# Kernel optimization log

Hardware: AMD Instinct MI355X
Metric: run time of the kernel (lower is better)

The kernel has to match this reference:

```python
import jax, jax.numpy as jnp
import numpy as np

N_NODES = 100000
N_EDGES = 1600000
D_IN = 64
D_OUT = 64
NUM_ETYPE = 2
NEG_SLOPE = 0.2


def setup_inputs() -> dict:
    key = jax.random.key(0)
    ks = jax.random.split(key, 9)
    feat = jax.random.normal(ks[0], (N_NODES, D_IN), dtype=jnp.float32)
    rel = jax.random.uniform(ks[1], (N_EDGES, NUM_ETYPE), dtype=jnp.float32)
    W_self = jax.random.normal(ks[2], (D_OUT, D_IN), dtype=jnp.float32) * 0.1
    b_self = jax.random.normal(ks[3], (D_OUT,), dtype=jnp.float32) * 0.1
    W_neigh = jax.random.normal(ks[4], (D_OUT, D_IN), dtype=jnp.float32) * 0.1
    b_neigh = jax.random.normal(ks[5], (D_OUT,), dtype=jnp.float32) * 0.1
    attn_e = jax.random.normal(ks[6], (NUM_ETYPE, 1), dtype=jnp.float32)
    src = jax.random.randint(ks[7], (N_EDGES,), 0, N_NODES, dtype=jnp.int32)
    dst = jax.random.randint(ks[8], (N_EDGES,), 0, N_NODES, dtype=jnp.int32)
    return {"feat": feat, "rel": rel, "W_self": W_self, "b_self": b_self,
            "W_neigh": W_neigh, "b_neigh": b_neigh, "attn_e": attn_e,
            "src": src, "dst": dst}


def reference(feat, rel, W_self, b_self, W_neigh, b_neigh, attn_e, src, dst):
    n = feat.shape[0]
    # per-edge attention score: [E, num_etype] @ [num_etype, 1] -> [E]
    e = jnp.squeeze(rel @ attn_e, axis=1)
    e = jax.nn.leaky_relu(e, negative_slope=NEG_SLOPE)
    # edge_softmax: segment softmax over edges grouped by destination node
    emax = jax.ops.segment_max(e, dst, num_segments=n)          # [N]
    ex = jnp.exp(e - emax[dst])                                  # [E]
    denom = jax.ops.segment_sum(ex, dst, num_segments=n)        # [N]
    a = ex / denom[dst]                                          # [E]
    # u_mul_e + sum aggregation: neigh[v] = sum_e a_e * feat[src_e]
    m = feat[src] * a[:, None]                                   # [E, D_IN]
    h_neigh = jax.ops.segment_sum(m, dst, num_segments=n)       # [N, D_IN]
    # rst = fc_self(h_self) + fc_neigh(h_neigh)  (torch Linear: x @ W.T + b)
    return feat @ W_self.T + b_self + h_neigh @ W_neigh.T + b_neigh
```

## Files before the change

### kernel.cpp

```cpp
#include <hip/hip_runtime.h>
#include <hip/hip_bf16.h>

#define N_NODES 100000
#define N_EDGES 1600000
#define D 64
#define NEG_SLOPE 0.2f

#define BSHIFT 10
#define BNODES 1024
#define NBUCK ((N_NODES + BNODES - 1) >> BSHIFT)
#define BUCKET_CAP 17408
#define P1_EPB 4096
#define P1_T 512
#define P1_IT (P1_EPB / P1_T)

__global__ __launch_bounds__(P1_T) void binning_kernel(
    const float2* __restrict__ rel, const float* __restrict__ attn_e,
    const int* __restrict__ src, const int* __restrict__ dst,
    int* __restrict__ bucket_cursor, uint2* __restrict__ binned)
{
    __shared__ uint2 staged1[P1_EPB];
    __shared__ uint2 staged2[P1_EPB];
    __shared__ int cnt[NBUCK];
    __shared__ int excl[NBUCK];
    __shared__ int chunkbase[NBUCK];

    int tid = threadIdx.x;
    int e0 = blockIdx.x * P1_EPB;
    int n = min(P1_EPB, N_EDGES - e0);

    for (int b = tid; b < NBUCK; b += P1_T) cnt[b] = 0;
    __syncthreads();

    float a0 = attn_e[0], a1 = attn_e[1];

    int myslot[P1_IT];
    #pragma unroll
    for (int j = 0; j < P1_IT; ++j) {
        int i = tid + j * P1_T;
        if (i < n) {
            int e = e0 + i;
            float2 r = rel[e];
            float sc = r.x * a0 + r.y * a1;
            sc = (sc > 0.f) ? sc : NEG_SLOPE * sc;
            float ev = __expf(sc);
            unsigned u = __float_as_uint(ev) + 0x8000u;
            unsigned wcode = (u >> 16) & 0x7FFFu;
            unsigned s = (unsigned)src[e];
            unsigned d = (unsigned)dst[e];
            staged1[i] = make_uint2((s << 15) | wcode, d);
            myslot[j] = atomicAdd(&cnt[d >> BSHIFT], 1);
        }
    }
    __syncthreads();
    if (tid == 0) {
        int run = 0;
        for (int b = 0; b < NBUCK; ++b) { excl[b] = run; run += cnt[b]; }
    }
    __syncthreads();
    #pragma unroll
    for (int j = 0; j < P1_IT; ++j) {
        int i = tid + j * P1_T;
        if (i < n) {
            uint2 v = staged1[i];
            staged2[excl[v.y >> BSHIFT] + myslot[j]] = v;
        }
    }
    if (tid < NBUCK)
        chunkbase[tid] = atomicAdd(&bucket_cursor[tid], cnt[tid]);
    __syncthreads();
    for (int i = tid; i < n; i += P1_T) {
        uint2 v = staged2[i];
        int b = (int)(v.y >> BSHIFT);
        binned[(size_t)b * BUCKET_CAP + chunkbase[b] + (i - excl[b])] = v;
    }
}

__global__ __launch_bounds__(1024) void csr_kernel(
    const int* __restrict__ bucket_cursor, const uint2* __restrict__ binned,
    int* __restrict__ offsets, unsigned* __restrict__ edata)
{
    __shared__ unsigned vals[BUCKET_CAP];
    __shared__ int hist[BNODES];
    __shared__ int nexcl[BNODES];
    __shared__ int cur[BNODES];
    __shared__ int bc[NBUCK];
    __shared__ int base_sh;

    int b = blockIdx.x;
    int tid = threadIdx.x;

    if (tid < NBUCK) bc[tid] = bucket_cursor[tid];
    hist[tid] = 0;
    cur[tid] = 0;
    __syncthreads();
    if (tid == 0) {
        int s = 0;
        for (int i = 0; i < b; ++i) s += bc[i];
        base_sh = s;
    }
    __syncthreads();
    int count = bc[b];
    int base = base_sh;
    const uint2* bin = binned + (size_t)b * BUCKET_CAP;

    for (int i = tid; i < count; i += 1024)
        atomicAdd(&hist[bin[i].y & (BNODES - 1)], 1);
    __syncthreads();

    int h = hist[tid];
    nexcl[tid] = h;
    __syncthreads();
    for (int d = 1; d < BNODES; d <<= 1) {
        int u = (tid >= d) ? nexcl[tid - d] : 0;
        __syncthreads();
        nexcl[tid] += u;
        __syncthreads();
    }
    int excl = nexcl[tid] - h;
    __syncthreads();
    nexcl[tid] = excl;
    __syncthreads();

    int node = (b << BSHIFT) + tid;
    if (node < N_NODES) offsets[node] = base + excl;
    if (b == NBUCK - 1 && tid == 0) offsets[N_NODES] = N_EDGES;

    for (int i = tid; i < count; i += 1024) {
        uint2 e = bin[i];
        int d = e.y & (BNODES - 1);
        int t = atomicAdd(&cur[d], 1);
        vals[nexcl[d] + t] = e.x;
    }
    __syncthreads();
    for (int i = tid; i < count; i += 1024)
        edata[base + i] = vals[i];
}

typedef __attribute__((ext_vector_type(8))) short bf16x8;
typedef __attribute__((ext_vector_type(4))) float f32x4;
#define MFMA16(a, b, c) __builtin_amdgcn_mfma_f32_16x16x32_bf16(a, b, c, 0, 0, 0)

__device__ __forceinline__ short bf16_rne(float f) {
    unsigned u = __float_as_uint(f);
    u += 0x7FFFu + ((u >> 16) & 1u);
    return (short)(u >> 16);
}
__device__ __forceinline__ float bf16_to_f(short h) {
    return __uint_as_float(((unsigned)(unsigned short)h) << 16);
}
__device__ __forceinline__ void cvt8(float4 f0, float4 f1,
                                     bf16x8& hi, bf16x8& lo) {
    float v[8] = {f0.x, f0.y, f0.z, f0.w, f1.x, f1.y, f1.z, f1.w};
    #pragma unroll
    for (int j = 0; j < 8; ++j) {
        short h = bf16_rne(v[j]);
        hi[j] = h;
        lo[j] = bf16_rne(v[j] - bf16_to_f(h));
    }
}

__global__ __launch_bounds__(512) void gemm_fused_kernel(
    const float* __restrict__ feat, const float* __restrict__ W_self,
    const float* __restrict__ W_neigh, const float* __restrict__ b_self,
    const float* __restrict__ b_neigh, float* __restrict__ out,
    __hip_bfloat16* __restrict__ g)
{
    int tid = threadIdx.x;
    int lane = tid & 63;
    int wave = tid >> 6;
    int llo = lane & 15;
    int lhi = lane >> 4;
    int rb = blockIdx.x * 128 + wave * 16;
    if (rb >= N_NODES) return;

    int arow = rb + llo;
    if (arow > N_NODES - 1) arow = N_NODES - 1;
    const float4* fr = (const float4*)(feat + (size_t)arow * D);
    bf16x8 ahi[2], alo[2];
    #pragma unroll
    for (int s = 0; s < 2; ++s)
        cvt8(fr[s * 8 + lhi * 2], fr[s * 8 + lhi * 2 + 1], ahi[s], alo[s]);

    unsigned short* g16 = (unsigned short*)g;
    #pragma unroll
    for (int nt = 0; nt < 4; ++nt) {
        int col = nt * 16 + llo;
        const float4* ws = (const float4*)(W_self + (size_t)col * D);
        const float4* wn = (const float4*)(W_neigh + (size_t)col * D);
        f32x4 accS = {0.f, 0.f, 0.f, 0.f};
        f32x4 accN = {0.f, 0.f, 0.f, 0.f};
        #pragma unroll
        for (int s = 0; s < 2; ++s) {
            bf16x8 bh, bl;
            cvt8(ws[s * 8 + lhi * 2], ws[s * 8 + lhi * 2 + 1], bh, bl);
            accS = MFMA16(ahi[s], bh, accS);
            accS = MFMA16(alo[s], bh, accS);
            accS = MFMA16(ahi[s], bl, accS);
            cvt8(wn[s * 8 + lhi * 2], wn[s * 8 + lhi * 2 + 1], bh, bl);
            accN = MFMA16(ahi[s], bh, accN);
            accN = MFMA16(alo[s], bh, accN);
            accN = MFMA16(ahi[s], bl, accN);
        }
        float bias = b_self[col] + b_neigh[col];
        #pragma unroll
        for (int rg = 0; rg < 4; ++rg) {
            int r = rb + lhi * 4 + rg;
            if (r < N_NODES) {
                out[(size_t)r * D + col] = accS[rg] + bias;
                g16[(size_t)r * D + col] = (unsigned short)bf16_rne(accN[rg]);
            }
        }
    }
}

__global__ __launch_bounds__(256) void aggregate_kernel(
    const uint* __restrict__ g32, const unsigned* __restrict__ edata,
    const int* __restrict__ offsets, float* __restrict__ out)
{
    int v = blockIdx.x * 4 + (threadIdx.x >> 6);
    int lane = threadIdx.x & 63;
    int q = lane >> 4;
    int t = lane & 15;
    int lo = offsets[v], hi = offsets[v + 1];
    float4 acc = make_float4(0.f, 0.f, 0.f, 0.f);
    float sum = 0.f;

    for (int i = lo; i < hi; i += 16) {
        int e0 = i + q;
        int e1 = i + 4 + q;
        int e2 = i + 8 + q;
        int e3 = i + 12 + q;
        int ec0 = (e0 < hi) ? e0 : hi - 1;
        int ec1 = (e1 < hi) ? e1 : hi - 1;
        int ec2 = (e2 < hi) ? e2 : hi - 1;
        int ec3 = (e3 < hi) ? e3 : hi - 1;
        unsigned p0 = edata[ec0];
        unsigned p1 = edata[ec1];
        unsigned p2 = edata[ec2];
        unsigned p3 = edata[ec3];
        float w0 = (e0 < hi) ? __uint_as_float((p0 & 0x7FFFu) << 16) : 0.f;
        float w1 = (e1 < hi) ? __uint_as_float((p1 & 0x7FFFu) << 16) : 0.f;
        float w2 = (e2 < hi) ? __uint_as_float((p2 & 0x7FFFu) << 16) : 0.f;
        float w3 = (e3 < hi) ? __uint_as_float((p3 & 0x7FFFu) << 16) : 0.f;
        const uint2* r0 = (const uint2*)(g32 + (size_t)(p0 >> 15) * (D / 2));
        const uint2* r1 = (const uint2*)(g32 + (size_t)(p1 >> 15) * (D / 2));
        const uint2* r2 = (const uint2*)(g32 + (size_t)(p2 >> 15) * (D / 2));
        const uint2* r3 = (const uint2*)(g32 + (size_t)(p3 >> 15) * (D / 2));
        uint2 u0 = r0[t];
        uint2 u1 = r1[t];
        uint2 u2 = r2[t];
        uint2 u3 = r3[t];
        acc.x += w0 * __uint_as_float(u0.x << 16);
        acc.y += w0 * __uint_as_float(u0.x & 0xFFFF0000u);
        acc.z += w0 * __uint_as_float(u0.y << 16);
        acc.w += w0 * __uint_as_float(u0.y & 0xFFFF0000u);
        sum += w0;
        acc.x += w1 * __uint_as_float(u1.x << 16);
        acc.y += w1 * __uint_as_float(u1.x & 0xFFFF0000u);
        acc.z += w1 * __uint_as_float(u1.y << 16);
        acc.w += w1 * __uint_as_float(u1.y & 0xFFFF0000u);
        sum += w1;
        acc.x += w2 * __uint_as_float(u2.x << 16);
        acc.y += w2 * __uint_as_float(u2.x & 0xFFFF0000u);
        acc.z += w2 * __uint_as_float(u2.y << 16);
        acc.w += w2 * __uint_as_float(u2.y & 0xFFFF0000u);
        sum += w2;
        acc.x += w3 * __uint_as_float(u3.x << 16);
        acc.y += w3 * __uint_as_float(u3.x & 0xFFFF0000u);
        acc.z += w3 * __uint_as_float(u3.y << 16);
        acc.w += w3 * __uint_as_float(u3.y & 0xFFFF0000u);
        sum += w3;
    }
    #pragma unroll
    for (int mm = 16; mm <= 32; mm <<= 1) {
        acc.x += __shfl_xor(acc.x, mm, 64);
        acc.y += __shfl_xor(acc.y, mm, 64);
        acc.z += __shfl_xor(acc.z, mm, 64);
        acc.w += __shfl_xor(acc.w, mm, 64);
        sum   += __shfl_xor(sum,   mm, 64);
    }
    if (hi > lo && q == 0) {
        float inv = 1.f / sum;
        float4* orow = (float4*)(out + (size_t)v * D);
        float4 c = orow[t];
        c.x += acc.x * inv; c.y += acc.y * inv;
        c.z += acc.z * inv; c.w += acc.w * inv;
        orow[t] = c;
    }
}

extern "C" void kernel_launch(void* const* d_in, const int* in_sizes, int n_in,
                              void* d_out, int out_size, void* d_ws, size_t ws_size,
                              hipStream_t stream) {
    const float* feat    = (const float*)d_in[0];
    const float* rel     = (const float*)d_in[1];
    const float* W_self  = (const float*)d_in[2];
    const float* b_self  = (const float*)d_in[3];
    const float* W_neigh = (const float*)d_in[4];
    const float* b_neigh = (const float*)d_in[5];
    const float* attn_e  = (const float*)d_in[6];
    const int*   src     = (const int*)d_in[7];
    const int*   dst     = (const int*)d_in[8];
    float* out = (float*)d_out;

    uint2* binned = (uint2*)d_ws;
    __hip_bfloat16* g = (__hip_bfloat16*)(binned + (size_t)NBUCK * BUCKET_CAP);
    unsigned* edata = (unsigned*)((char*)g + (size_t)N_NODES * D * 2);
    int* offsets = (int*)(edata + N_EDGES);
    int* bucket_cursor = offsets + N_NODES + 1;

    hipMemsetAsync(bucket_cursor, 0, NBUCK * sizeof(int), stream);

    binning_kernel<<<(N_EDGES + P1_EPB - 1) / P1_EPB, P1_T, 0, stream>>>(
        (const float2*)rel, attn_e, src, dst, bucket_cursor, binned);
    csr_kernel<<<NBUCK, 1024, 0, stream>>>(
        bucket_cursor, binned, offsets, edata);
    gemm_fused_kernel<<<(N_NODES + 127) / 128, 512, 0, stream>>>(
        feat, W_self, W_neigh, b_self, b_neigh, out, g);
    aggregate_kernel<<<N_NODES / 4, 256, 0, stream>>>(
        (const uint*)g, edata, offsets, out);
}
```

Before: 206.8 us.

## Precompute bf16 weight fragments once, transpose GEMM output mapping, shrink CSR buckets

An extra block in the binning kernel converts W_self and W_neigh into hi/lo bf16 MFMA fragments a single time and sums the two biases into one vector. Before this, every GEMM wave reloaded and converted the weights itself. The GEMM swaps the MFMA operand roles so each lane holds four consecutive output columns of one node, which lets it write float4 and packed bf16 stores instead of scalar ones. It also halves the block size. Separately, the bucket size drops from 1024 to 512 nodes, giving the CSR kernel more blocks, each with less shared memory. The cost is that only half the threads do work in the CSR prefix scan.

Result: faster. 189.8 us (-8.2%).

```diff
diff --git a/kernel.cpp b/kernel.cpp
--- a/kernel.cpp
+++ b/kernel.cpp
@@ -6,18 +6,45 @@
 #define D 64
 #define NEG_SLOPE 0.2f
 
-#define BSHIFT 10
-#define BNODES 1024
+#define BSHIFT 9
+#define BNODES 512
 #define NBUCK ((N_NODES + BNODES - 1) >> BSHIFT)
-#define BUCKET_CAP 17408
+#define BUCKET_CAP 8896
 #define P1_EPB 4096
 #define P1_T 512
 #define P1_IT (P1_EPB / P1_T)
+#define GRID_BIN ((N_EDGES + P1_EPB - 1) / P1_EPB)
+
+typedef __attribute__((ext_vector_type(8))) short bf16x8;
+typedef __attribute__((ext_vector_type(4))) float f32x4;
+#define MFMA16(a, b, c) __builtin_amdgcn_mfma_f32_16x16x32_bf16(a, b, c, 0, 0, 0)
+
+__device__ __forceinline__ short bf16_rne(float f) {
+    unsigned u = __float_as_uint(f);
+    u += 0x7FFFu + ((u >> 16) & 1u);
+    return (short)(u >> 16);
+}
+__device__ __forceinline__ float bf16_to_f(short h) {
+    return __uint_as_float(((unsigned)(unsigned short)h) << 16);
+}
+__device__ __forceinline__ void cvt8(float4 f0, float4 f1,
+                                     bf16x8& hi, bf16x8& lo) {
+    float v[8] = {f0.x, f0.y, f0.z, f0.w, f1.x, f1.y, f1.z, f1.w};
+    #pragma unroll
+    for (int j = 0; j < 8; ++j) {
+        short h = bf16_rne(v[j]);
+        hi[j] = h;
+        lo[j] = bf16_rne(v[j] - bf16_to_f(h));
+    }
+}
 
 __global__ __launch_bounds__(P1_T) void binning_kernel(
     const float2* __restrict__ rel, const float* __restrict__ attn_e,
     const int* __restrict__ src, const int* __restrict__ dst,
-    int* __restrict__ bucket_cursor, uint2* __restrict__ binned)
+    int* __restrict__ bucket_cursor, uint2* __restrict__ binned,
+    const float* __restrict__ W_self, const float* __restrict__ W_neigh,
+    const float* __restrict__ b_self, const float* __restrict__ b_neigh,
+    bf16x8* __restrict__ wfrag, float* __restrict__ bsum)
 {
     __shared__ uint2 staged1[P1_EPB];
     __shared__ uint2 staged2[P1_EPB];
@@ -26,6 +53,27 @@
     __shared__ int chunkbase[NBUCK];
 
     int tid = threadIdx.x;
+
+    if (blockIdx.x == GRID_BIN) {
+        if (tid < D) bsum[tid] = b_self[tid] + b_neigh[tid];
+        for (int c = tid; c < 1024; c += P1_T) {
+            int nt = c >> 8;
+            int mat = (c >> 7) & 1;
+            int s = (c >> 6) & 1;
+            int lane = c & 63;
+            const float* Wm = mat ? W_neigh : W_self;
+            int row = nt * 16 + (lane & 15);
+            int koff = s * 32 + (lane >> 4) * 8;
+            const float4* p = (const float4*)(Wm + row * D + koff);
+            bf16x8 hi, lo;
+            cvt8(p[0], p[1], hi, lo);
+            int base = (c >> 6) * 128 + (c & 63);
+            wfrag[base] = hi;
+            wfrag[base + 64] = lo;
+        }
+        return;
+    }
+
     int e0 = blockIdx.x * P1_EPB;
     int n = min(P1_EPB, N_EDGES - e0);
 
@@ -91,8 +139,7 @@
     int tid = threadIdx.x;
 
     if (tid < NBUCK) bc[tid] = bucket_cursor[tid];
-    hist[tid] = 0;
-    cur[tid] = 0;
+    if (tid < BNODES) { hist[tid] = 0; cur[tid] = 0; }
     __syncthreads();
     if (tid == 0) {
         int s = 0;
@@ -108,22 +155,23 @@
         atomicAdd(&hist[bin[i].y & (BNODES - 1)], 1);
     __syncthreads();
 
-    int h = hist[tid];
-    nexcl[tid] = h;
+    int h = 0;
+    if (tid < BNODES) { h = hist[tid]; nexcl[tid] = h; }
     __syncthreads();
     for (int d = 1; d < BNODES; d <<= 1) {
-        int u = (tid >= d) ? nexcl[tid - d] : 0;
+        int u = (tid >= d && tid < BNODES) ? nexcl[tid - d] : 0;
         __syncthreads();
-        nexcl[tid] += u;
+        if (tid < BNODES) nexcl[tid] += u;
         __syncthreads();
     }
-    int excl = nexcl[tid] - h;
-    __syncthreads();
-    nexcl[tid] = excl;
+    int excl = 0;
+    if (tid < BNODES) excl = nexcl[tid] - h;
+    __syncthreads();
+    if (tid < BNODES) nexcl[tid] = excl;
     __syncthreads();
 
     int node = (b << BSHIFT) + tid;
-    if (node < N_NODES) offsets[node] = base + excl;
+    if (tid < BNODES && node < N_NODES) offsets[node] = base + excl;
     if (b == NBUCK - 1 && tid == 0) offsets[N_NODES] = N_EDGES;
 
     for (int i = tid; i < count; i += 1024) {
@@ -137,33 +185,9 @@
         edata[base + i] = vals[i];
 }
 
-typedef __attribute__((ext_vector_type(8))) short bf16x8;
-typedef __attribute__((ext_vector_type(4))) float f32x4;
-#define MFMA16(a, b, c) __builtin_amdgcn_mfma_f32_16x16x32_bf16(a, b, c, 0, 0, 0)
-
-__device__ __forceinline__ short bf16_rne(float f) {
-    unsigned u = __float_as_uint(f);
-    u += 0x7FFFu + ((u >> 16) & 1u);
-    return (short)(u >> 16);
-}
-__device__ __forceinline__ float bf16_to_f(short h) {
-    return __uint_as_float(((unsigned)(unsigned short)h) << 16);
-}
-__device__ __forceinline__ void cvt8(float4 f0, float4 f1,
-                                     bf16x8& hi, bf16x8& lo) {
-    float v[8] = {f0.x, f0.y, f0.z, f0.w, f1.x, f1.y, f1.z, f1.w};
-    #pragma unroll
-    for (int j = 0; j < 8; ++j) {
-        short h = bf16_rne(v[j]);
-        hi[j] = h;
-        lo[j] = bf16_rne(v[j] - bf16_to_f(h));
-    }
-}
-
-__global__ __launch_bounds__(512) void gemm_fused_kernel(
-    const float* __restrict__ feat, const float* __restrict__ W_self,
-    const float* __restrict__ W_neigh, const float* __restrict__ b_self,
-    const float* __restrict__ b_neigh, float* __restrict__ out,
+__global__ __launch_bounds__(256) void gemm_fused_kernel(
+    const float* __restrict__ feat, const bf16x8* __restrict__ wfrag,
+    const float* __restrict__ bsum, float* __restrict__ out,
     __hip_bfloat16* __restrict__ g)
 {
     int tid = threadIdx.x;
@@ -171,45 +195,61 @@
     int wave = tid >> 6;
     int llo = lane & 15;
     int lhi = lane >> 4;
-    int rb = blockIdx.x * 128 + wave * 16;
+    int rb = blockIdx.x * 64 + wave * 16;
     if (rb >= N_NODES) return;
 
-    int arow = rb + llo;
-    if (arow > N_NODES - 1) arow = N_NODES - 1;
-    const float4* fr = (const float4*)(feat + (size_t)arow * D);
-    bf16x8 ahi[2], alo[2];
+    int node = rb + llo;
+    bool valid = node < N_NODES;
+    int nclamp = valid ? node : N_NODES - 1;
+    const float4* fr = (const float4*)(feat + (size_t)nclamp * D);
+    bf16x8 fhi[2], flo[2];
     #pragma unroll
     for (int s = 0; s < 2; ++s)
-        cvt8(fr[s * 8 + lhi * 2], fr[s * 8 + lhi * 2 + 1], ahi[s], alo[s]);
-
+        cvt8(fr[s * 8 + lhi * 2], fr[s * 8 + lhi * 2 + 1], fhi[s], flo[s]);
+
+    const float4* bs4 = (const float4*)bsum;
     unsigned short* g16 = (unsigned short*)g;
+
     #pragma unroll
     for (int nt = 0; nt < 4; ++nt) {
-        int col = nt * 16 + llo;
-        const float4* ws = (const float4*)(W_self + (size_t)col * D);
-        const float4* wn = (const float4*)(W_neigh + (size_t)col * D);
+        int base = nt * 512 + lane;
+        bf16x8 wSh0 = wfrag[base];
+        bf16x8 wSl0 = wfrag[base + 64];
+        bf16x8 wSh1 = wfrag[base + 128];
+        bf16x8 wSl1 = wfrag[base + 192];
+        bf16x8 wNh0 = wfrag[base + 256];
+        bf16x8 wNl0 = wfrag[base + 320];
+        bf16x8 wNh1 = wfrag[base + 384];
+        bf16x8 wNl1 = wfrag[base + 448];
         f32x4 accS = {0.f, 0.f, 0.f, 0.f};
         f32x4 accN = {0.f, 0.f, 0.f, 0.f};
-        #pragma unroll
-        for (int s = 0; s < 2; ++s) {
-            bf16x8 bh, bl;
-            cvt8(ws[s * 8 + lhi * 2], ws[s * 8 + lhi * 2 + 1], bh, bl);
-            accS = MFMA16(ahi[s], bh, accS);
-            accS = MFMA16(alo[s], bh, accS);
-            accS = MFMA16(ahi[s], bl, accS);
-            cvt8(wn[s * 8 + lhi * 2], wn[s * 8 + lhi * 2 + 1], bh, bl);
-            accN = MFMA16(ahi[s], bh, accN);
-            accN = MFMA16(alo[s], bh, accN);
-            accN = MFMA16(ahi[s], bl, accN);
-        }
-        float bias = b_self[col] + b_neigh[col];
-        #pragma unroll
-        for (int rg = 0; rg < 4; ++rg) {
-            int r = rb + lhi * 4 + rg;
-            if (r < N_NODES) {
-                out[(size_t)r * D + col] = accS[rg] + bias;
-                g16[(size_t)r * D + col] = (unsigned short)bf16_rne(accN[rg]);
-            }
+        accS = MFMA16(wSh0, fhi[0], accS);
+        accN = MFMA16(wNh0, fhi[0], accN);
+        accS = MFMA16(wSl0, fhi[0], accS);
+        accN = MFMA16(wNl0, fhi[0], accN);
+        accS = MFMA16(wSh0, flo[0], accS);
+        accN = MFMA16(wNh0, flo[0], accN);
+        accS = MFMA16(wSh1, fhi[1], accS);
+        accN = MFMA16(wNh1, fhi[1], accN);
+        accS = MFMA16(wSl1, fhi[1], accS);
+        accN = MFMA16(wNl1, fhi[1], accN);
+        accS = MFMA16(wSh1, flo[1], accS);
+        accN = MFMA16(wNh1, flo[1], accN);
+
+        if (valid) {
+            float4 bb = bs4[nt * 4 + lhi];
+            float4 o;
+            o.x = accS[0] + bb.x;
+            o.y = accS[1] + bb.y;
+            o.z = accS[2] + bb.z;
+            o.w = accS[3] + bb.w;
+            *(float4*)(out + (size_t)node * D + nt * 16 + lhi * 4) = o;
+            uint2 gp;
+            gp.x = (unsigned)(unsigned short)bf16_rne(accN[0])
+                 | ((unsigned)(unsigned short)bf16_rne(accN[1]) << 16);
+            gp.y = (unsigned)(unsigned short)bf16_rne(accN[2])
+                 | ((unsigned)(unsigned short)bf16_rne(accN[3]) << 16);
+            *(uint2*)(g16 + (size_t)node * D + nt * 16 + lhi * 4) = gp;
         }
     }
 }
@@ -307,17 +347,20 @@
     uint2* binned = (uint2*)d_ws;
     __hip_bfloat16* g = (__hip_bfloat16*)(binned + (size_t)NBUCK * BUCKET_CAP);
     unsigned* edata = (unsigned*)((char*)g + (size_t)N_NODES * D * 2);
-    int* offsets = (int*)(edata + N_EDGES);
+    bf16x8* wfrag = (bf16x8*)(edata + N_EDGES);
+    float* bsum = (float*)(wfrag + 2048);
+    int* offsets = (int*)(bsum + 64);
     int* bucket_cursor = offsets + N_NODES + 1;
 
     hipMemsetAsync(bucket_cursor, 0, NBUCK * sizeof(int), stream);
 
-    binning_kernel<<<(N_EDGES + P1_EPB - 1) / P1_EPB, P1_T, 0, stream>>>(
-        (const float2*)rel, attn_e, src, dst, bucket_cursor, binned);
+    binning_kernel<<<GRID_BIN + 1, P1_T, 0, stream>>>(
+        (const float2*)rel, attn_e, src, dst, bucket_cursor, binned,
+        W_self, W_neigh, b_self, b_neigh, wfrag, bsum);
     csr_kernel<<<NBUCK, 1024, 0, stream>>>(
         bucket_cursor, binned, offsets, edata);
-    gemm_fused_kernel<<<(N_NODES + 127) / 128, 512, 0, stream>>>(
-        feat, W_self, W_neigh, b_self, b_neigh, out, g);
+    gemm_fused_kernel<<<(N_NODES + 63) / 64, 256, 0, stream>>>(
+        feat, wfrag, bsum, out, g);
     aggregate_kernel<<<N_NODES / 4, 256, 0, stream>>>(
         (const uint*)g, edata, offsets, out);
 }
```
